# Optimization experiments

Measured on AMD Instinct MI355X. Metric: run time of the kernel, lower is better.

The kernel has to match this reference:

```python
import jax, jax.numpy as jnp
import numpy as np
from jax.scipy.special import logsumexp

S, L = 32768, 512  # seq_len, label_num


def setup_inputs() -> dict:
    key = jax.random.key(0)
    k1, k2, k3 = jax.random.split(key, 3)
    logit = jax.random.normal(k1, (S, L), dtype=jnp.float32)   # emissions [S, L]
    labels = jax.random.randint(k2, (S,), 0, L)                # gold path [S]
    T = jax.random.normal(k3, (L, L), dtype=jnp.float32)       # T[next, prev]
    return {"logit": logit, "labels": labels, "T": T}


def _crf_loss(logit, T, labels):
    # Forward algorithm: alpha_t[j] = logsumexp_i(alpha_{t-1}[i] + T[j, i]) + feat_t[j]
    alpha0 = logit[0]

    def step(alpha, feat):
        new_alpha = logsumexp(alpha[None, :] + T, axis=1) + feat  # [L]
        return new_alpha, None

    alpha_final, _ = jax.lax.scan(step, alpha0, logit[1:])
    log_Z = logsumexp(alpha_final)

    # Gold path score: feat_0[y0] + sum_{t>0} (feat_t[y_t] + T[y_t, y_{t-1}])
    emit = logit[0, labels[0]] + jnp.sum(logit[jnp.arange(1, logit.shape[0]), labels[1:]])
    trans = jnp.sum(T[labels[1:], labels[:-1]])
    gold = emit + trans
    return log_Z - gold


def reference(logit, labels, T):
    return _crf_loss(logit, T, labels)
```

## Files before the change

### kernel.cpp

```cpp
#include <hip/hip_runtime.h>
#include <stdint.h>


#define S_LEN 32768
#define L 512
#define CH 16
#define NCF 2048
#define NB  256
#define TPB 1024
#define LN448 6.104793232f
#define LN2   0.6931471806f

#define OFF_EAF  0
#define OFF_EAB  (256*1024)
#define OFF_G    (512*1024)
#define OFF_H    (OFF_G + 2048*512*2)
#define OFF_LSE  (OFF_H + 2048*512*2)
#define OFF_GOLD (OFF_LSE + 4104*4)
#define OFF_BAR  (OFF_GOLD + 1024)

#define PL_OFF   0
#define SP_OFF   16384
#define SR_OFF   17664
#define LF_OFF   18432
#define SMEM_TOTAL (18432 + 3*32768)

typedef float v4f __attribute__((ext_vector_type(4)));

__device__ __forceinline__ float b2f(unsigned short u){
  return __uint_as_float(((unsigned)u) << 16);
}
__device__ __forceinline__ unsigned short f2b(float x){
  unsigned u = __float_as_uint(x);
  return (unsigned short)((u + 0x7fffu + ((u >> 16) & 1u)) >> 16);
}
__device__ __forceinline__ unsigned char to_fp8(float v){
  int u = __builtin_amdgcn_cvt_pk_fp8_f32(v, v, 0, false);
  return (unsigned char)(u & 0xff);
}

__device__ __forceinline__ void stg_u8(unsigned char* p, unsigned char v){
  __hip_atomic_store(p, v, __ATOMIC_RELAXED, __HIP_MEMORY_SCOPE_AGENT);
}
__device__ __forceinline__ void stg_u64(unsigned long long* p, unsigned long long v){
  __hip_atomic_store(p, v, __ATOMIC_RELAXED, __HIP_MEMORY_SCOPE_AGENT);
}
__device__ __forceinline__ void stg_f32(float* p, float v){
  __hip_atomic_store(p, v, __ATOMIC_RELAXED, __HIP_MEMORY_SCOPE_AGENT);
}

__device__ __forceinline__ void gl2lds16(const void* g, void* l){
  __builtin_amdgcn_global_load_lds(
      (const __attribute__((address_space(1))) void*)g,
      (__attribute__((address_space(3))) void*)l, 16, 0, 0);
}

__device__ __forceinline__ void lds_sync(){
  asm volatile("s_waitcnt lgkmcnt(0)" ::: "memory");
  __builtin_amdgcn_sched_barrier(0);
  __builtin_amdgcn_s_barrier();
  __builtin_amdgcn_sched_barrier(0);
}
__device__ __forceinline__ void step_sync(){
  asm volatile("s_waitcnt vmcnt(2) lgkmcnt(0)" ::: "memory");
  __builtin_amdgcn_sched_barrier(0);
  __builtin_amdgcn_s_barrier();
  __builtin_amdgcn_sched_barrier(0);
}

__device__ __forceinline__ void grid_bar(unsigned* bar, unsigned target){
  __syncthreads();
  if (threadIdx.x == 0) {
    __hip_atomic_fetch_add(bar, 1u, __ATOMIC_RELAXED, __HIP_MEMORY_SCOPE_AGENT);
    unsigned it = 0;
    while (__hip_atomic_load(bar, __ATOMIC_RELAXED, __HIP_MEMORY_SCOPE_AGENT) < target) {
      __builtin_amdgcn_s_sleep(8);
      if ((++it & 255u) == 0u)
        (void)__hip_atomic_load(bar, __ATOMIC_ACQUIRE, __HIP_MEMORY_SCOPE_AGENT);
    }
    __builtin_amdgcn_fence(__ATOMIC_ACQUIRE, "agent");
  }
  __syncthreads();
}

__device__ __forceinline__ float blockSum(float v, float* sred){
  #pragma unroll
  for (int off = 32; off >= 1; off >>= 1) v += __shfl_xor(v, off);
  int wid = threadIdx.x >> 6, lane = threadIdx.x & 63;
  if (lane == 0) sred[wid] = v;
  __syncthreads();
  if (threadIdx.x < 16) {
    float t = sred[threadIdx.x];
    t += __shfl_xor(t, 8); t += __shfl_xor(t, 4);
    t += __shfl_xor(t, 2); t += __shfl_xor(t, 1);
    if (threadIdx.x == 0) sred[16] = t;
  }
  __syncthreads();
  float r = sred[16];
  __syncthreads();
  return r;
}

__device__ __forceinline__ float waveMax(float v){
  #pragma unroll
  for (int off = 32; off >= 1; off >>= 1) v = fmaxf(v, __shfl_xor(v, off));
  return v;
}
__device__ __forceinline__ float waveSum(float v){
  #pragma unroll
  for (int off = 32; off >= 1; off >>= 1) v += __shfl_xor(v, off);
  return v;
}

extern "C" __global__ __launch_bounds__(TPB, 4)
void crf_fused(const float* __restrict__ logit,
               const int* __restrict__ labels,
               const float* __restrict__ T,
               float* __restrict__ out,
               unsigned char* __restrict__ EAf,
               unsigned char* __restrict__ EAb,
               unsigned short* __restrict__ G,
               unsigned short* __restrict__ H,
               float* __restrict__ lsebuf,
               float* __restrict__ part,
               unsigned* __restrict__ bar){
  extern __shared__ __align__(16) char smem[];
  unsigned char* Pl = (unsigned char*)(smem + PL_OFF);
  float (*sPart)[20] = (float(*)[20])(smem + SP_OFF);
  float* sredG       = (float*)(smem + SR_OFF);
  char*  LF          = smem + LF_OFF;

  const int tidx = threadIdx.x;

  {
    int tid = blockIdx.x*TPB + tidx;
    int r    = tid & 7;
    int lane = (tid >> 3) & 63;
    int kt   = (tid >> 9) & 15;
    int R16  = tid >> 13;
    int j = R16*16 + (lane & 15);
    int i = kt*32 + ((lane >> 4) << 3) + r;
    stg_u8(EAf + tid, to_fp8(2.0f * __expf(T[j*L + i])));
    stg_u8(EAb + tid, to_fp8(2.0f * __expf(T[i*L + j])));
  }
  {
    float acc = 0.f;
    if (tidx < 128) {
      int t = blockIdx.x*128 + tidx;
      int yt = labels[t];
      float v = logit[(size_t)t*L + yt];
      if (t > 0) v += T[yt*L + labels[t-1]];
      acc = v;
    }
    float s = blockSum(acc, sredG);
    if (tidx == 0) stg_f32(part + blockIdx.x, s);
  }
  grid_bar(bar, NB);

  {
    const int w    = tidx >> 6;
    const int lane = tidx & 63;
    const int quad = lane >> 4;
    const int cl   = lane & 15;
    const bool fwd = (blockIdx.x < NB/2);
    const int  b   = fwd ? blockIdx.x : (blockIdx.x - NB/2);
    const int  cg  = fwd ? (b*16 + cl) : (1 + b*16 + cl);
    const int  cgc = min(cg, NCF-1);
    const bool isc0 = fwd && (cg == 0);
    const int  jrow0 = w*32 + quad*4;

    const int  cgw  = fwd ? (b*16 + w) : (1 + b*16 + w);
    const int  cgcw = min(cgw, NCF-1);
    const unsigned swzw = (unsigned)((w & 7) << 4);
    const unsigned so   = ((unsigned)(lane*16)) ^ swzw;

    const long* EAp = (const long*)(fwd ? EAf : EAb);
    long eA[2][16];
    #pragma unroll
    for (int mt = 0; mt < 2; ++mt)
      #pragma unroll
      for (int kt = 0; kt < 16; ++kt)
        eA[mt][kt] = EAp[(((w*2 + mt)*16) + kt)*64 + lane];

    int pladdr0, pladdr1;
    {
      int r0 = jrow0;
      pladdr0 = (r0 >> 5)*512 + ((((r0 >> 3) & 3)*16 + cl) << 3) + (r0 & 7);
      r0 = jrow0 + 16;
      pladdr1 = (r0 >> 5)*512 + ((((r0 >> 3) & 3)*16 + cl) << 3) + (r0 & 7);
    }
    const int bbbase = lane*8;
    const int scl = (cl & 7) << 4;
    const int ib  = w*128 + quad*16;
    const int fa0 = cl*2048 + (ib ^ scl);
    const int fa1 = cl*2048 + ((ib + 64) ^ scl);

    {
      size_t t0 = (size_t)(fwd ? (cgcw*CH + 0) : (cgcw*CH + CH - 2 - 0));
      size_t t1 = (size_t)(fwd ? (cgcw*CH + 1) : (cgcw*CH + CH - 2 - 1));
      const char* r0p = (const char*)logit + t0*(L*4);
      const char* r1p = (const char*)logit + t1*(L*4);
      char* d0 = LF + 0*32768 + w*2048;
      char* d1 = LF + 1*32768 + w*2048;
      gl2lds16(r0p + so, d0);  gl2lds16(r0p + 1024 + so, d0 + 1024);
      gl2lds16(r1p + so, d1);  gl2lds16(r1p + 1024 + so, d1 + 1024);
    }

    v4f v0, v1;
    if (fwd) {
      v0 = (v4f){1.f,1.f,1.f,1.f}; v1 = v0;
    } else {
      const float* ip = logit + (size_t)(cgc*CH + CH - 1)*L + jrow0;
      float4 x0 = *(const float4*)ip, x1 = *(const float4*)(ip + 16);
      v0 = (v4f){__expf(x0.x),__expf(x0.y),__expf(x0.z),__expf(x0.w)};
      v1 = (v4f){__expf(x1.x),__expf(x1.y),__expf(x1.z),__expf(x1.w)};
    }
    float m = 0.0f;
    int par = 0;
    int bo0 = 0, bo1 = 32768, bo2 = 2*32768;

    {
      float mx = fmaxf(fmaxf(fmaxf(v0[0],v0[1]),fmaxf(v0[2],v0[3])),
                       fmaxf(fmaxf(v1[0],v1[1]),fmaxf(v1[2],v1[3])));
      mx = fmaxf(mx, __shfl_xor(mx, 16));
      mx = fmaxf(mx, __shfl_xor(mx, 32));
      if (quad == 0) sPart[cl][w] = mx;
      lds_sync();
      const float4* sp4 = (const float4*)&sPart[cl][0];
      float4 q0 = sp4[0], q1 = sp4[1], q2 = sp4[2], q3 = sp4[3];
      float M = fmaxf(fmaxf(fmaxf(fmaxf(q0.x,q0.y),fmaxf(q0.z,q0.w)),
                            fmaxf(fmaxf(q1.x,q1.y),fmaxf(q1.z,q1.w))),
                      fmaxf(fmaxf(fmaxf(q2.x,q2.y),fmaxf(q2.z,q2.w)),
                            fmaxf(fmaxf(q3.x,q3.y),fmaxf(q3.z,q3.w))));
      float sc = 448.0f / M;
      int u0 = __builtin_amdgcn_cvt_pk_fp8_f32(v0[0]*sc, v0[1]*sc, 0, false);
      u0     = __builtin_amdgcn_cvt_pk_fp8_f32(v0[2]*sc, v0[3]*sc, u0, true);
      *(int*)&Pl[pladdr0] = u0;
      int u1 = __builtin_amdgcn_cvt_pk_fp8_f32(v1[0]*sc, v1[1]*sc, 0, false);
      u1     = __builtin_amdgcn_cvt_pk_fp8_f32(v1[2]*sc, v1[3]*sc, u1, true);
      *(int*)&Pl[pladdr1] = u1;
      m = __logf(M) - LN448;
      step_sync();
    }

    for (int k = 0; k < CH; ++k) {
      const bool last = (k == CH-1);
      const bool useF = fwd || !last;

      {
        const int ks = k + 2;
        const bool ok = fwd ? (ks <= CH-1) : (ks <= CH-2);
        if (ok) {
          size_t t = (size_t)(fwd ? (cgcw*CH + ks) : (cgcw*CH + CH - 2 - ks));
          const char* row = (const char*)logit + t*(L*4);
          char* dst = LF + bo2 + w*2048;
          gl2lds16(row + so, dst);
          gl2lds16(row + 1024 + so, dst + 1024);
        }
      }

      v4f a0 = (v4f){0.f,0.f,0.f,0.f};
      v4f a1 = (v4f){0.f,0.f,0.f,0.f};
      {
        const unsigned char* plr = Pl + par*8192 + bbbase;
        #pragma unroll
        for (int kt = 0; kt < 16; ++kt) {
          long bb = *(const long*)(plr + kt*512);
          a0 = __builtin_amdgcn_mfma_f32_16x16x32_fp8_fp8(eA[0][kt], bb, a0, 0, 0, 0);
          a1 = __builtin_amdgcn_mfma_f32_16x16x32_fp8_fp8(eA[1][kt], bb, a1, 0, 0, 0);
        }
      }

      if (useF) {
        const char* fb = LF + bo0;
        float4 q0 = *(const float4*)(fb + fa0);
        float4 q1 = *(const float4*)(fb + fa1);
        float f0=__expf(q0.x), f1=__expf(q0.y), f2=__expf(q0.z), f3=__expf(q0.w);
        float g0=__expf(q1.x), g1=__expf(q1.y), g2=__expf(q1.z), g3=__expf(q1.w);
        a0 = (v4f){a0[0]*f0, a0[1]*f1, a0[2]*f2, a0[3]*f3};
        a1 = (v4f){a1[0]*g0, a1[1]*g1, a1[2]*g2, a1[3]*g3};
        if (k == 0 && isc0) {
          a0 = (v4f){f0,f1,f2,f3}; a1 = (v4f){g0,g1,g2,g3}; m = 0.0f;
        }
      }

      if (last) {
        if (cg <= NCF-1) {
          float madj = m - (isc0 ? (float)(CH-1) : (float)CH) * LN2;
          unsigned short* dst = (fwd ? G : H) + (size_t)cg*L + jrow0;
          unsigned long long pv =
               (unsigned long long)f2b(__logf(a0[0]) + madj)
            | ((unsigned long long)f2b(__logf(a0[1]) + madj) << 16)
            | ((unsigned long long)f2b(__logf(a0[2]) + madj) << 32)
            | ((unsigned long long)f2b(__logf(a0[3]) + madj) << 48);
          stg_u64((unsigned long long*)dst, pv);
          pv = (unsigned long long)f2b(__logf(a1[0]) + madj)
            | ((unsigned long long)f2b(__logf(a1[1]) + madj) << 16)
            | ((unsigned long long)f2b(__logf(a1[2]) + madj) << 32)
            | ((unsigned long long)f2b(__logf(a1[3]) + madj) << 48);
          stg_u64((unsigned long long*)(dst + 16), pv);
        }
      } else {
        float mx = fmaxf(fmaxf(fmaxf(a0[0],a0[1]),fmaxf(a0[2],a0[3])),
                         fmaxf(fmaxf(a1[0],a1[1]),fmaxf(a1[2],a1[3])));
        mx = fmaxf(mx, __shfl_xor(mx, 16));
        mx = fmaxf(mx, __shfl_xor(mx, 32));
        if (quad == 0) sPart[cl][w] = mx;
        lds_sync();
        const float4* sp4 = (const float4*)&sPart[cl][0];
        float4 q0 = sp4[0], q1 = sp4[1], q2 = sp4[2], q3 = sp4[3];
        float M = fmaxf(fmaxf(fmaxf(fmaxf(q0.x,q0.y),fmaxf(q0.z,q0.w)),
                              fmaxf(fmaxf(q1.x,q1.y),fmaxf(q1.z,q1.w))),
                        fmaxf(fmaxf(fmaxf(q2.x,q2.y),fmaxf(q2.z,q2.w)),
                              fmaxf(fmaxf(q3.x,q3.y),fmaxf(q3.z,q3.w))));
        float sc = 448.0f / M;
        int u0 = __builtin_amdgcn_cvt_pk_fp8_f32(a0[0]*sc, a0[1]*sc, 0, false);
        u0     = __builtin_amdgcn_cvt_pk_fp8_f32(a0[2]*sc, a0[3]*sc, u0, true);
        *(int*)&Pl[(par^1)*8192 + pladdr0] = u0;
        int u1 = __builtin_amdgcn_cvt_pk_fp8_f32(a1[0]*sc, a1[1]*sc, 0, false);
        u1     = __builtin_amdgcn_cvt_pk_fp8_f32(a1[2]*sc, a1[3]*sc, u1, true);
        *(int*)&Pl[(par^1)*8192 + pladdr1] = u1;
        m += __logf(M) - LN448;
        step_sync();
        par ^= 1;
        int tmp = bo0; bo0 = bo1; bo1 = bo2; bo2 = tmp;
      }
    }
  }
  grid_bar(bar, 2*NB);

  if (blockIdx.x < 128) {
    const int w    = tidx >> 6;
    const int lane = tidx & 63;
    const int g    = blockIdx.x*16 + w;
    const int j8   = lane*8;
    if (g == 0) {
      const unsigned short* p = G + (size_t)(NCF-1)*L + j8;
      ushort4 a = *(const ushort4*)p, bq = *(const ushort4*)(p + 4);
      float v[8] = { b2f(a.x),b2f(a.y),b2f(a.z),b2f(a.w),
                     b2f(bq.x),b2f(bq.y),b2f(bq.z),b2f(bq.w) };
      float mx = v[0];
      #pragma unroll
      for (int r = 1; r < 8; ++r) mx = fmaxf(mx, v[r]);
      mx = waveMax(mx);
      float s = 0.f;
      #pragma unroll
      for (int r = 0; r < 8; ++r) s += __expf(v[r] - mx);
      s = waveSum(s);
      if (lane == 0) stg_f32(lsebuf + 2*NCF, mx + __logf(s));
    } else {
      const unsigned short* hp = H + (size_t)g*L + j8;
      const unsigned short* gp = G + (size_t)(g-1)*L + j8;
      ushort4 ha = *(const ushort4*)hp, hb = *(const ushort4*)(hp + 4);
      ushort4 ga = *(const ushort4*)gp, gb = *(const ushort4*)(gp + 4);
      float hv[8] = { b2f(ha.x),b2f(ha.y),b2f(ha.z),b2f(ha.w),
                      b2f(hb.x),b2f(hb.y),b2f(hb.z),b2f(hb.w) };
      float gv[8] = { b2f(ga.x),b2f(ga.y),b2f(ga.z),b2f(ga.w),
                      b2f(gb.x),b2f(gb.y),b2f(gb.z),b2f(gb.w) };
      float m1 = -3.0e38f, m2 = -3.0e38f;
      #pragma unroll
      for (int r = 0; r < 8; ++r) {
        float a = hv[r] + gv[r];
        m1 = fmaxf(m1, a); m2 = fmaxf(m2, hv[r]);
      }
      m1 = waveMax(m1); m2 = waveMax(m2);
      float s1 = 0.f, s2 = 0.f;
      #pragma unroll
      for (int r = 0; r < 8; ++r) {
        s1 += __expf(hv[r] + gv[r] - m1);
        s2 += __expf(hv[r] - m2);
      }
      s1 = waveSum(s1); s2 = waveSum(s2);
      if (lane == 0) {
        stg_f32(lsebuf + g,       m1 + __logf(s1));
        stg_f32(lsebuf + NCF + g, m2 + __logf(s2));
      }
    }
  }
  grid_bar(bar, 3*NB);

  if (blockIdx.x == 0) {
    float acc = 0.f;
    for (int c = tidx; c < NCF; c += TPB)
      if (c >= 1) acc += lsebuf[c] - lsebuf[NCF + c];
    if (tidx < NB) acc -= part[tidx];
    float s = blockSum(acc, sredG);
    if (tidx == 0) out[0] = lsebuf[2*NCF] + s;
  }
}

extern "C" void kernel_launch(void* const* d_in, const int* in_sizes, int n_in,
                              void* d_out, int out_size, void* d_ws, size_t ws_size,
                              hipStream_t stream){
  const float* logit = (const float*)d_in[0];
  const int* labels  = (const int*)d_in[1];
  const float* T     = (const float*)d_in[2];
  char* ws = (char*)d_ws;

  static bool attr_set = false;
  if (!attr_set) {
    hipFuncSetAttribute((const void*)crf_fused,
                        hipFuncAttributeMaxDynamicSharedMemorySize, SMEM_TOTAL);
    attr_set = true;
  }

  hipMemsetAsync(ws + OFF_BAR, 0, 64, stream);
  crf_fused<<<NB, TPB, SMEM_TOTAL, stream>>>(
      logit, labels, T, (float*)d_out,
      (unsigned char*)(ws + OFF_EAF), (unsigned char*)(ws + OFF_EAB),
      (unsigned short*)(ws + OFF_G), (unsigned short*)(ws + OFF_H),
      (float*)(ws + OFF_LSE), (float*)(ws + OFF_GOLD),
      (unsigned*)(ws + OFF_BAR));
}
```

Before: 156.5 us.

## Split persistent fused kernel into four launches, replacing software grid barriers

Breaks the single persistent kernel, which had atomic-spin grid barriers, into four kernels: prep, chunk scan, per-chunk LSE and final reduction. Stream ordering now provides the synchronisation, so the barrier memset, the spin loops and the agent-scope atomic stores go away in favour of plain stores. The cost is three extra launch gaps, and the chunk kernel has to reload its inputs from global memory in a fresh launch.

```diff
diff --git a/kernel.cpp b/kernel.cpp
--- a/kernel.cpp
+++ b/kernel.cpp
@@ -17,11 +17,9 @@
 #define OFF_H    (OFF_G + 2048*512*2)
 #define OFF_LSE  (OFF_H + 2048*512*2)
 #define OFF_GOLD (OFF_LSE + 4104*4)
-#define OFF_BAR  (OFF_GOLD + 1024)
 
 #define PL_OFF   0
 #define SP_OFF   16384
-#define SR_OFF   17664
 #define LF_OFF   18432
 #define SMEM_TOTAL (18432 + 3*32768)
 
@@ -37,16 +35,6 @@
 __device__ __forceinline__ unsigned char to_fp8(float v){
   int u = __builtin_amdgcn_cvt_pk_fp8_f32(v, v, 0, false);
   return (unsigned char)(u & 0xff);
-}
-
-__device__ __forceinline__ void stg_u8(unsigned char* p, unsigned char v){
-  __hip_atomic_store(p, v, __ATOMIC_RELAXED, __HIP_MEMORY_SCOPE_AGENT);
-}
-__device__ __forceinline__ void stg_u64(unsigned long long* p, unsigned long long v){
-  __hip_atomic_store(p, v, __ATOMIC_RELAXED, __HIP_MEMORY_SCOPE_AGENT);
-}
-__device__ __forceinline__ void stg_f32(float* p, float v){
-  __hip_atomic_store(p, v, __ATOMIC_RELAXED, __HIP_MEMORY_SCOPE_AGENT);
 }
 
 __device__ __forceinline__ void gl2lds16(const void* g, void* l){
@@ -68,22 +56,18 @@
   __builtin_amdgcn_sched_barrier(0);
 }
 
-__device__ __forceinline__ void grid_bar(unsigned* bar, unsigned target){
-  __syncthreads();
-  if (threadIdx.x == 0) {
-    __hip_atomic_fetch_add(bar, 1u, __ATOMIC_RELAXED, __HIP_MEMORY_SCOPE_AGENT);
-    unsigned it = 0;
-    while (__hip_atomic_load(bar, __ATOMIC_RELAXED, __HIP_MEMORY_SCOPE_AGENT) < target) {
-      __builtin_amdgcn_s_sleep(8);
-      if ((++it & 255u) == 0u)
-        (void)__hip_atomic_load(bar, __ATOMIC_ACQUIRE, __HIP_MEMORY_SCOPE_AGENT);
-    }
-    __builtin_amdgcn_fence(__ATOMIC_ACQUIRE, "agent");
-  }
-  __syncthreads();
-}
-
-__device__ __forceinline__ float blockSum(float v, float* sred){
+__device__ __forceinline__ float waveMax(float v){
+  #pragma unroll
+  for (int off = 32; off >= 1; off >>= 1) v = fmaxf(v, __shfl_xor(v, off));
+  return v;
+}
+__device__ __forceinline__ float waveSum(float v){
+  #pragma unroll
+  for (int off = 32; off >= 1; off >>= 1) v += __shfl_xor(v, off);
+  return v;
+}
+
+__device__ __forceinline__ float blockSum16(float v, float* sred){
   #pragma unroll
   for (int off = 32; off >= 1; off >>= 1) v += __shfl_xor(v, off);
   int wid = threadIdx.x >> 6, lane = threadIdx.x & 63;
@@ -100,38 +84,32 @@
   __syncthreads();
   return r;
 }
-
-__device__ __forceinline__ float waveMax(float v){
-  #pragma unroll
-  for (int off = 32; off >= 1; off >>= 1) v = fmaxf(v, __shfl_xor(v, off));
-  return v;
-}
-__device__ __forceinline__ float waveSum(float v){
+__device__ __forceinline__ float blockSum8(float v, float* sred){
   #pragma unroll
   for (int off = 32; off >= 1; off >>= 1) v += __shfl_xor(v, off);
-  return v;
-}
-
-extern "C" __global__ __launch_bounds__(TPB, 4)
-void crf_fused(const float* __restrict__ logit,
-               const int* __restrict__ labels,
-               const float* __restrict__ T,
-               float* __restrict__ out,
-               unsigned char* __restrict__ EAf,
-               unsigned char* __restrict__ EAb,
-               unsigned short* __restrict__ G,
-               unsigned short* __restrict__ H,
-               float* __restrict__ lsebuf,
-               float* __restrict__ part,
-               unsigned* __restrict__ bar){
-  extern __shared__ __align__(16) char smem[];
-  unsigned char* Pl = (unsigned char*)(smem + PL_OFF);
-  float (*sPart)[20] = (float(*)[20])(smem + SP_OFF);
-  float* sredG       = (float*)(smem + SR_OFF);
-  char*  LF          = smem + LF_OFF;
-
+  int wid = threadIdx.x >> 6, lane = threadIdx.x & 63;
+  if (lane == 0) sred[wid] = v;
+  __syncthreads();
+  if (threadIdx.x < 8) {
+    float t = sred[threadIdx.x];
+    t += __shfl_xor(t, 4); t += __shfl_xor(t, 2); t += __shfl_xor(t, 1);
+    if (threadIdx.x == 0) sred[8] = t;
+  }
+  __syncthreads();
+  float r = sred[8];
+  __syncthreads();
+  return r;
+}
+
+extern "C" __global__ __launch_bounds__(TPB)
+void crf_prep(const float* __restrict__ logit,
+              const int* __restrict__ labels,
+              const float* __restrict__ T,
+              unsigned char* __restrict__ EAf,
+              unsigned char* __restrict__ EAb,
+              float* __restrict__ part){
+  __shared__ float sredG[17];
   const int tidx = threadIdx.x;
-
   {
     int tid = blockIdx.x*TPB + tidx;
     int r    = tid & 7;
@@ -140,8 +118,8 @@
     int R16  = tid >> 13;
     int j = R16*16 + (lane & 15);
     int i = kt*32 + ((lane >> 4) << 3) + r;
-    stg_u8(EAf + tid, to_fp8(2.0f * __expf(T[j*L + i])));
-    stg_u8(EAb + tid, to_fp8(2.0f * __expf(T[i*L + j])));
+    EAf[tid] = to_fp8(2.0f * __expf(T[j*L + i]));
+    EAb[tid] = to_fp8(2.0f * __expf(T[i*L + j]));
   }
   {
     float acc = 0.f;
@@ -152,76 +130,168 @@
       if (t > 0) v += T[yt*L + labels[t-1]];
       acc = v;
     }
-    float s = blockSum(acc, sredG);
-    if (tidx == 0) stg_f32(part + blockIdx.x, s);
-  }
-  grid_bar(bar, NB);
-
+    float s = blockSum16(acc, sredG);
+    if (tidx == 0) part[blockIdx.x] = s;
+  }
+}
+
+extern "C" __global__ __launch_bounds__(TPB, 4)
+void crf_chunks(const float* __restrict__ logit,
+                const unsigned char* __restrict__ EAf,
+                const unsigned char* __restrict__ EAb,
+                unsigned short* __restrict__ G,
+                unsigned short* __restrict__ H){
+  extern __shared__ __align__(16) char smem[];
+  unsigned char* Pl  = (unsigned char*)(smem + PL_OFF);
+  float (*sPart)[20] = (float(*)[20])(smem + SP_OFF);
+  char*  LF          = smem + LF_OFF;
+
+  const int tidx = threadIdx.x;
+  const int w    = tidx >> 6;
+  const int lane = tidx & 63;
+  const int quad = lane >> 4;
+  const int cl   = lane & 15;
+  const bool fwd = (blockIdx.x < NB/2);
+  const int  b   = fwd ? blockIdx.x : (blockIdx.x - NB/2);
+  const int  cg  = fwd ? (b*16 + cl) : (1 + b*16 + cl);
+  const int  cgc = min(cg, NCF-1);
+  const bool isc0 = fwd && (cg == 0);
+  const int  jrow0 = w*32 + quad*4;
+
+  const int  cgw  = fwd ? (b*16 + w) : (1 + b*16 + w);
+  const int  cgcw = min(cgw, NCF-1);
+  const unsigned swzw = (unsigned)((w & 7) << 4);
+  const unsigned so   = ((unsigned)(lane*16)) ^ swzw;
+
+  const long* EAp = (const long*)(fwd ? EAf : EAb);
+  long eA[2][16];
+  #pragma unroll
+  for (int mt = 0; mt < 2; ++mt)
+    #pragma unroll
+    for (int kt = 0; kt < 16; ++kt)
+      eA[mt][kt] = EAp[(((w*2 + mt)*16) + kt)*64 + lane];
+
+  int pladdr0, pladdr1;
   {
-    const int w    = tidx >> 6;
-    const int lane = tidx & 63;
-    const int quad = lane >> 4;
-    const int cl   = lane & 15;
-    const bool fwd = (blockIdx.x < NB/2);
-    const int  b   = fwd ? blockIdx.x : (blockIdx.x - NB/2);
-    const int  cg  = fwd ? (b*16 + cl) : (1 + b*16 + cl);
-    const int  cgc = min(cg, NCF-1);
-    const bool isc0 = fwd && (cg == 0);
-    const int  jrow0 = w*32 + quad*4;
-
-    const int  cgw  = fwd ? (b*16 + w) : (1 + b*16 + w);
-    const int  cgcw = min(cgw, NCF-1);
-    const unsigned swzw = (unsigned)((w & 7) << 4);
-    const unsigned so   = ((unsigned)(lane*16)) ^ swzw;
-
-    const long* EAp = (const long*)(fwd ? EAf : EAb);
-    long eA[2][16];
-    #pragma unroll
-    for (int mt = 0; mt < 2; ++mt)
+    int r0 = jrow0;
+    pladdr0 = (r0 >> 5)*512 + ((((r0 >> 3) & 3)*16 + cl) << 3) + (r0 & 7);
+    r0 = jrow0 + 16;
+    pladdr1 = (r0 >> 5)*512 + ((((r0 >> 3) & 3)*16 + cl) << 3) + (r0 & 7);
+  }
+  const int bbbase = lane*8;
+  const int scl = (cl & 7) << 4;
+  const int ib  = w*128 + quad*16;
+  const int fa0 = cl*2048 + (ib ^ scl);
+  const int fa1 = cl*2048 + ((ib + 64) ^ scl);
+
+  {
+    size_t t0 = (size_t)(fwd ? (cgcw*CH + 0) : (cgcw*CH + CH - 2 - 0));
+    size_t t1 = (size_t)(fwd ? (cgcw*CH + 1) : (cgcw*CH + CH - 2 - 1));
+    const char* r0p = (const char*)logit + t0*(L*4);
+    const char* r1p = (const char*)logit + t1*(L*4);
+    char* d0 = LF + 0*32768 + w*2048;
+    char* d1 = LF + 1*32768 + w*2048;
+    gl2lds16(r0p + so, d0);  gl2lds16(r0p + 1024 + so, d0 + 1024);
+    gl2lds16(r1p + so, d1);  gl2lds16(r1p + 1024 + so, d1 + 1024);
+  }
+
+  v4f v0, v1;
+  if (fwd) {
+    v0 = (v4f){1.f,1.f,1.f,1.f}; v1 = v0;
+  } else {
+    const float* ip = logit + (size_t)(cgc*CH + CH - 1)*L + jrow0;
+    float4 x0 = *(const float4*)ip, x1 = *(const float4*)(ip + 16);
+    v0 = (v4f){__expf(x0.x),__expf(x0.y),__expf(x0.z),__expf(x0.w)};
+    v1 = (v4f){__expf(x1.x),__expf(x1.y),__expf(x1.z),__expf(x1.w)};
+  }
+  float m = 0.0f;
+  int par = 0;
+  int bo0 = 0, bo1 = 32768, bo2 = 2*32768;
+
+  {
+    float mx = fmaxf(fmaxf(fmaxf(v0[0],v0[1]),fmaxf(v0[2],v0[3])),
+                     fmaxf(fmaxf(v1[0],v1[1]),fmaxf(v1[2],v1[3])));
+    mx = fmaxf(mx, __shfl_xor(mx, 16));
+    mx = fmaxf(mx, __shfl_xor(mx, 32));
+    if (quad == 0) sPart[cl][w] = mx;
+    lds_sync();
+    const float4* sp4 = (const float4*)&sPart[cl][0];
+    float4 q0 = sp4[0], q1 = sp4[1], q2 = sp4[2], q3 = sp4[3];
+    float M = fmaxf(fmaxf(fmaxf(fmaxf(q0.x,q0.y),fmaxf(q0.z,q0.w)),
+                          fmaxf(fmaxf(q1.x,q1.y),fmaxf(q1.z,q1.w))),
+                    fmaxf(fmaxf(fmaxf(q2.x,q2.y),fmaxf(q2.z,q2.w)),
+                          fmaxf(fmaxf(q3.x,q3.y),fmaxf(q3.z,q3.w))));
+    float sc = 448.0f / M;
+    int u0 = __builtin_amdgcn_cvt_pk_fp8_f32(v0[0]*sc, v0[1]*sc, 0, false);
+    u0     = __builtin_amdgcn_cvt_pk_fp8_f32(v0[2]*sc, v0[3]*sc, u0, true);
+    *(int*)&Pl[pladdr0] = u0;
+    int u1 = __builtin_amdgcn_cvt_pk_fp8_f32(v1[0]*sc, v1[1]*sc, 0, false);
+    u1     = __builtin_amdgcn_cvt_pk_fp8_f32(v1[2]*sc, v1[3]*sc, u1, true);
+    *(int*)&Pl[pladdr1] = u1;
+    m = __logf(M) - LN448;
+    step_sync();
+  }
+
+  for (int k = 0; k < CH; ++k) {
+    const bool last = (k == CH-1);
+    const bool useF = fwd || !last;
+
+    {
+      const int ks = k + 2;
+      const bool ok = fwd ? (ks <= CH-1) : (ks <= CH-2);
+      if (ok) {
+        size_t t = (size_t)(fwd ? (cgcw*CH + ks) : (cgcw*CH + CH - 2 - ks));
+        const char* row = (const char*)logit + t*(L*4);
+        char* dst = LF + bo2 + w*2048;
+        gl2lds16(row + so, dst);
+        gl2lds16(row + 1024 + so, dst + 1024);
+      }
+    }
+
+    v4f a0 = (v4f){0.f,0.f,0.f,0.f};
+    v4f a1 = (v4f){0.f,0.f,0.f,0.f};
+    {
+      const unsigned char* plr = Pl + par*8192 + bbbase;
       #pragma unroll
-      for (int kt = 0; kt < 16; ++kt)
-        eA[mt][kt] = EAp[(((w*2 + mt)*16) + kt)*64 + lane];
-
-    int pladdr0, pladdr1;
-    {
-      int r0 = jrow0;
-      pladdr0 = (r0 >> 5)*512 + ((((r0 >> 3) & 3)*16 + cl) << 3) + (r0 & 7);
-      r0 = jrow0 + 16;
-      pladdr1 = (r0 >> 5)*512 + ((((r0 >> 3) & 3)*16 + cl) << 3) + (r0 & 7);
-    }
-    const int bbbase = lane*8;
-    const int scl = (cl & 7) << 4;
-    const int ib  = w*128 + quad*16;
-    const int fa0 = cl*2048 + (ib ^ scl);
-    const int fa1 = cl*2048 + ((ib + 64) ^ scl);
-
-    {
-      size_t t0 = (size_t)(fwd ? (cgcw*CH + 0) : (cgcw*CH + CH - 2 - 0));
-      size_t t1 = (size_t)(fwd ? (cgcw*CH + 1) : (cgcw*CH + CH - 2 - 1));
-      const char* r0p = (const char*)logit + t0*(L*4);
-      const char* r1p = (const char*)logit + t1*(L*4);
-      char* d0 = LF + 0*32768 + w*2048;
-      char* d1 = LF + 1*32768 + w*2048;
-      gl2lds16(r0p + so, d0);  gl2lds16(r0p + 1024 + so, d0 + 1024);
-      gl2lds16(r1p + so, d1);  gl2lds16(r1p + 1024 + so, d1 + 1024);
-    }
-
-    v4f v0, v1;
-    if (fwd) {
-      v0 = (v4f){1.f,1.f,1.f,1.f}; v1 = v0;
+      for (int kt = 0; kt < 16; ++kt) {
+        long bb = *(const long*)(plr + kt*512);
+        a0 = __builtin_amdgcn_mfma_f32_16x16x32_fp8_fp8(eA[0][kt], bb, a0, 0, 0, 0);
+        a1 = __builtin_amdgcn_mfma_f32_16x16x32_fp8_fp8(eA[1][kt], bb, a1, 0, 0, 0);
+      }
+    }
+
+    if (useF) {
+      const char* fb = LF + bo0;
+      float4 q0 = *(const float4*)(fb + fa0);
+      float4 q1 = *(const float4*)(fb + fa1);
+      float f0=__expf(q0.x), f1=__expf(q0.y), f2=__expf(q0.z), f3=__expf(q0.w);
+      float g0=__expf(q1.x), g1=__expf(q1.y), g2=__expf(q1.z), g3=__expf(q1.w);
+      a0 = (v4f){a0[0]*f0, a0[1]*f1, a0[2]*f2, a0[3]*f3};
+      a1 = (v4f){a1[0]*g0, a1[1]*g1, a1[2]*g2, a1[3]*g3};
+      if (k == 0 && isc0) {
+        a0 = (v4f){f0,f1,f2,f3}; a1 = (v4f){g0,g1,g2,g3}; m = 0.0f;
+      }
+    }
+
+    if (last) {
+      if (cg <= NCF-1) {
+        float madj = m - (isc0 ? (float)(CH-1) : (float)CH) * LN2;
+        unsigned short* dst = (fwd ? G : H) + (size_t)cg*L + jrow0;
+        unsigned long long pv =
+             (unsigned long long)f2b(__logf(a0[0]) + madj)
+          | ((unsigned long long)f2b(__logf(a0[1]) + madj) << 16)
+          | ((unsigned long long)f2b(__logf(a0[2]) + madj) << 32)
+          | ((unsigned long long)f2b(__logf(a0[3]) + madj) << 48);
+        *(unsigned long long*)dst = pv;
+        pv = (unsigned long long)f2b(__logf(a1[0]) + madj)
+          | ((unsigned long long)f2b(__logf(a1[1]) + madj) << 16)
+          | ((unsigned long long)f2b(__logf(a1[2]) + madj) << 32)
+          | ((unsigned long long)f2b(__logf(a1[3]) + madj) << 48);
+        *(unsigned long long*)(dst + 16) = pv;
+      }
     } else {
-      const float* ip = logit + (size_t)(cgc*CH + CH - 1)*L + jrow0;
-      float4 x0 = *(const float4*)ip, x1 = *(const float4*)(ip + 16);
-      v0 = (v4f){__expf(x0.x),__expf(x0.y),__expf(x0.z),__expf(x0.w)};
-      v1 = (v4f){__expf(x1.x),__expf(x1.y),__expf(x1.z),__expf(x1.w)};
-    }
-    float m = 0.0f;
-    int par = 0;
-    int bo0 = 0, bo1 = 32768, bo2 = 2*32768;
-
-    {
-      float mx = fmaxf(fmaxf(fmaxf(v0[0],v0[1]),fmaxf(v0[2],v0[3])),
-                       fmaxf(fmaxf(v1[0],v1[1]),fmaxf(v1[2],v1[3])));
+      float mx = fmaxf(fmaxf(fmaxf(a0[0],a0[1]),fmaxf(a0[2],a0[3])),
+                       fmaxf(fmaxf(a1[0],a1[1]),fmaxf(a1[2],a1[3])));
       mx = fmaxf(mx, __shfl_xor(mx, 16));
       mx = fmaxf(mx, __shfl_xor(mx, 32));
       if (quad == 0) sPart[cl][w] = mx;
@@ -233,160 +303,86 @@
                       fmaxf(fmaxf(fmaxf(q2.x,q2.y),fmaxf(q2.z,q2.w)),
                             fmaxf(fmaxf(q3.x,q3.y),fmaxf(q3.z,q3.w))));
       float sc = 448.0f / M;
-      int u0 = __builtin_amdgcn_cvt_pk_fp8_f32(v0[0]*sc, v0[1]*sc, 0, false);
-      u0     = __builtin_amdgcn_cvt_pk_fp8_f32(v0[2]*sc, v0[3]*sc, u0, true);
-      *(int*)&Pl[pladdr0] = u0;
-      int u1 = __builtin_amdgcn_cvt_pk_fp8_f32(v1[0]*sc, v1[1]*sc, 0, false);
-      u1     = __builtin_amdgcn_cvt_pk_fp8_f32(v1[2]*sc, v1[3]*sc, u1, true);
-      *(int*)&Pl[pladdr1] = u1;
-      m = __logf(M) - LN448;
+      int u0 = __builtin_amdgcn_cvt_pk_fp8_f32(a0[0]*sc, a0[1]*sc, 0, false);
+      u0     = __builtin_amdgcn_cvt_pk_fp8_f32(a0[2]*sc, a0[3]*sc, u0, true);
+      *(int*)&Pl[(par^1)*8192 + pladdr0] = u0;
+      int u1 = __builtin_amdgcn_cvt_pk_fp8_f32(a1[0]*sc, a1[1]*sc, 0, false);
+      u1     = __builtin_amdgcn_cvt_pk_fp8_f32(a1[2]*sc, a1[3]*sc, u1, true);
+      *(int*)&Pl[(par^1)*8192 + pladdr1] = u1;
+      m += __logf(M) - LN448;
       step_sync();
-    }
-
-    for (int k = 0; k < CH; ++k) {
-      const bool last = (k == CH-1);
-      const bool useF = fwd || !last;
-
-      {
-        const int ks = k + 2;
-        const bool ok = fwd ? (ks <= CH-1) : (ks <= CH-2);
-        if (ok) {
-          size_t t = (size_t)(fwd ? (cgcw*CH + ks) : (cgcw*CH + CH - 2 - ks));
-          const char* row = (const char*)logit + t*(L*4);
-          char* dst = LF + bo2 + w*2048;
-          gl2lds16(row + so, dst);
-          gl2lds16(row + 1024 + so, dst + 1024);
-        }
-      }
-
-      v4f a0 = (v4f){0.f,0.f,0.f,0.f};
-      v4f a1 = (v4f){0.f,0.f,0.f,0.f};
-      {
-        const unsigned char* plr = Pl + par*8192 + bbbase;
-        #pragma unroll
-        for (int kt = 0; kt < 16; ++kt) {
-          long bb = *(const long*)(plr + kt*512);
-          a0 = __builtin_amdgcn_mfma_f32_16x16x32_fp8_fp8(eA[0][kt], bb, a0, 0, 0, 0);
-          a1 = __builtin_amdgcn_mfma_f32_16x16x32_fp8_fp8(eA[1][kt], bb, a1, 0, 0, 0);
-        }
-      }
-
-      if (useF) {
-        const char* fb = LF + bo0;
-        float4 q0 = *(const float4*)(fb + fa0);
-        float4 q1 = *(const float4*)(fb + fa1);
-        float f0=__expf(q0.x), f1=__expf(q0.y), f2=__expf(q0.z), f3=__expf(q0.w);
-        float g0=__expf(q1.x), g1=__expf(q1.y), g2=__expf(q1.z), g3=__expf(q1.w);
-        a0 = (v4f){a0[0]*f0, a0[1]*f1, a0[2]*f2, a0[3]*f3};
-        a1 = (v4f){a1[0]*g0, a1[1]*g1, a1[2]*g2, a1[3]*g3};
-        if (k == 0 && isc0) {
-          a0 = (v4f){f0,f1,f2,f3}; a1 = (v4f){g0,g1,g2,g3}; m = 0.0f;
-        }
-      }
-
-      if (last) {
-        if (cg <= NCF-1) {
-          float madj = m - (isc0 ? (float)(CH-1) : (float)CH) * LN2;
-          unsigned short* dst = (fwd ? G : H) + (size_t)cg*L + jrow0;
-          unsigned long long pv =
-               (unsigned long long)f2b(__logf(a0[0]) + madj)
-            | ((unsigned long long)f2b(__logf(a0[1]) + madj) << 16)
-            | ((unsigned long long)f2b(__logf(a0[2]) + madj) << 32)
-            | ((unsigned long long)f2b(__logf(a0[3]) + madj) << 48);
-          stg_u64((unsigned long long*)dst, pv);
-          pv = (unsigned long long)f2b(__logf(a1[0]) + madj)
-            | ((unsigned long long)f2b(__logf(a1[1]) + madj) << 16)
-            | ((unsigned long long)f2b(__logf(a1[2]) + madj) << 32)
-            | ((unsigned long long)f2b(__logf(a1[3]) + madj) << 48);
-          stg_u64((unsigned long long*)(dst + 16), pv);
-        }
-      } else {
-        float mx = fmaxf(fmaxf(fmaxf(a0[0],a0[1]),fmaxf(a0[2],a0[3])),
-                         fmaxf(fmaxf(a1[0],a1[1]),fmaxf(a1[2],a1[3])));
-        mx = fmaxf(mx, __shfl_xor(mx, 16));
-        mx = fmaxf(mx, __shfl_xor(mx, 32));
-        if (quad == 0) sPart[cl][w] = mx;
-        lds_sync();
-        const float4* sp4 = (const float4*)&sPart[cl][0];
-        float4 q0 = sp4[0], q1 = sp4[1], q2 = sp4[2], q3 = sp4[3];
-        float M = fmaxf(fmaxf(fmaxf(fmaxf(q0.x,q0.y),fmaxf(q0.z,q0.w)),
-                              fmaxf(fmaxf(q1.x,q1.y),fmaxf(q1.z,q1.w))),
-                        fmaxf(fmaxf(fmaxf(q2.x,q2.y),fmaxf(q2.z,q2.w)),
-                              fmaxf(fmaxf(q3.x,q3.y),fmaxf(q3.z,q3.w))));
-        float sc = 448.0f / M;
-        int u0 = __builtin_amdgcn_cvt_pk_fp8_f32(a0[0]*sc, a0[1]*sc, 0, false);
-        u0     = __builtin_amdgcn_cvt_pk_fp8_f32(a0[2]*sc, a0[3]*sc, u0, true);
-        *(int*)&Pl[(par^1)*8192 + pladdr0] = u0;
-        int u1 = __builtin_amdgcn_cvt_pk_fp8_f32(a1[0]*sc, a1[1]*sc, 0, false);
-        u1     = __builtin_amdgcn_cvt_pk_fp8_f32(a1[2]*sc, a1[3]*sc, u1, true);
-        *(int*)&Pl[(par^1)*8192 + pladdr1] = u1;
-        m += __logf(M) - LN448;
-        step_sync();
-        par ^= 1;
-        int tmp = bo0; bo0 = bo1; bo1 = bo2; bo2 = tmp;
-      }
-    }
-  }
-  grid_bar(bar, 2*NB);
-
-  if (blockIdx.x < 128) {
-    const int w    = tidx >> 6;
-    const int lane = tidx & 63;
-    const int g    = blockIdx.x*16 + w;
-    const int j8   = lane*8;
-    if (g == 0) {
-      const unsigned short* p = G + (size_t)(NCF-1)*L + j8;
-      ushort4 a = *(const ushort4*)p, bq = *(const ushort4*)(p + 4);
-      float v[8] = { b2f(a.x),b2f(a.y),b2f(a.z),b2f(a.w),
-                     b2f(bq.x),b2f(bq.y),b2f(bq.z),b2f(bq.w) };
-      float mx = v[0];
-      #pragma unroll
-      for (int r = 1; r < 8; ++r) mx = fmaxf(mx, v[r]);
-      mx = waveMax(mx);
-      float s = 0.f;
-      #pragma unroll
-      for (int r = 0; r < 8; ++r) s += __expf(v[r] - mx);
-      s = waveSum(s);
-      if (lane == 0) stg_f32(lsebuf + 2*NCF, mx + __logf(s));
-    } else {
-      const unsigned short* hp = H + (size_t)g*L + j8;
-      const unsigned short* gp = G + (size_t)(g-1)*L + j8;
-      ushort4 ha = *(const ushort4*)hp, hb = *(const ushort4*)(hp + 4);
-      ushort4 ga = *(const ushort4*)gp, gb = *(const ushort4*)(gp + 4);
-      float hv[8] = { b2f(ha.x),b2f(ha.y),b2f(ha.z),b2f(ha.w),
-                      b2f(hb.x),b2f(hb.y),b2f(hb.z),b2f(hb.w) };
-      float gv[8] = { b2f(ga.x),b2f(ga.y),b2f(ga.z),b2f(ga.w),
-                      b2f(gb.x),b2f(gb.y),b2f(gb.z),b2f(gb.w) };
-      float m1 = -3.0e38f, m2 = -3.0e38f;
-      #pragma unroll
-      for (int r = 0; r < 8; ++r) {
-        float a = hv[r] + gv[r];
-        m1 = fmaxf(m1, a); m2 = fmaxf(m2, hv[r]);
-      }
-      m1 = waveMax(m1); m2 = waveMax(m2);
-      float s1 = 0.f, s2 = 0.f;
-      #pragma unroll
-      for (int r = 0; r < 8; ++r) {
-        s1 += __expf(hv[r] + gv[r] - m1);
-        s2 += __expf(hv[r] - m2);
-      }
-      s1 = waveSum(s1); s2 = waveSum(s2);
-      if (lane == 0) {
-        stg_f32(lsebuf + g,       m1 + __logf(s1));
-        stg_f32(lsebuf + NCF + g, m2 + __logf(s2));
-      }
-    }
-  }
-  grid_bar(bar, 3*NB);
-
-  if (blockIdx.x == 0) {
-    float acc = 0.f;
-    for (int c = tidx; c < NCF; c += TPB)
-      if (c >= 1) acc += lsebuf[c] - lsebuf[NCF + c];
-    if (tidx < NB) acc -= part[tidx];
-    float s = blockSum(acc, sredG);
-    if (tidx == 0) out[0] = lsebuf[2*NCF] + s;
-  }
+      par ^= 1;
+      int tmp = bo0; bo0 = bo1; bo1 = bo2; bo2 = tmp;
+    }
+  }
+}
+
+extern "C" __global__ __launch_bounds__(512)
+void crf_lse(const unsigned short* __restrict__ G,
+             const unsigned short* __restrict__ H,
+             float* __restrict__ lsebuf){
+  const int tidx = threadIdx.x;
+  const int w    = tidx >> 6;
+  const int lane = tidx & 63;
+  const int g    = blockIdx.x*8 + w;
+  const int j8   = lane*8;
+  if (g == 0) {
+    const unsigned short* p = G + (size_t)(NCF-1)*L + j8;
+    ushort4 a = *(const ushort4*)p, bq = *(const ushort4*)(p + 4);
+    float v[8] = { b2f(a.x),b2f(a.y),b2f(a.z),b2f(a.w),
+                   b2f(bq.x),b2f(bq.y),b2f(bq.z),b2f(bq.w) };
+    float mx = v[0];
+    #pragma unroll
+    for (int r = 1; r < 8; ++r) mx = fmaxf(mx, v[r]);
+    mx = waveMax(mx);
+    float s = 0.f;
+    #pragma unroll
+    for (int r = 0; r < 8; ++r) s += __expf(v[r] - mx);
+    s = waveSum(s);
+    if (lane == 0) lsebuf[2*NCF] = mx + __logf(s);
+  } else {
+    const unsigned short* hp = H + (size_t)g*L + j8;
+    const unsigned short* gp = G + (size_t)(g-1)*L + j8;
+    ushort4 ha = *(const ushort4*)hp, hb = *(const ushort4*)(hp + 4);
+    ushort4 ga = *(const ushort4*)gp, gb = *(const ushort4*)(gp + 4);
+    float hv[8] = { b2f(ha.x),b2f(ha.y),b2f(ha.z),b2f(ha.w),
+                    b2f(hb.x),b2f(hb.y),b2f(hb.z),b2f(hb.w) };
+    float gv[8] = { b2f(ga.x),b2f(ga.y),b2f(ga.z),b2f(ga.w),
+                    b2f(gb.x),b2f(gb.y),b2f(gb.z),b2f(gb.w) };
+    float m1 = -3.0e38f, m2 = -3.0e38f;
+    #pragma unroll
+    for (int r = 0; r < 8; ++r) {
+      float a = hv[r] + gv[r];
+      m1 = fmaxf(m1, a); m2 = fmaxf(m2, hv[r]);
+    }
+    m1 = waveMax(m1); m2 = waveMax(m2);
+    float s1 = 0.f, s2 = 0.f;
+    #pragma unroll
+    for (int r = 0; r < 8; ++r) {
+      s1 += __expf(hv[r] + gv[r] - m1);
+      s2 += __expf(hv[r] - m2);
+    }
+    s1 = waveSum(s1); s2 = waveSum(s2);
+    if (lane == 0) {
+      lsebuf[g]       = m1 + __logf(s1);
+      lsebuf[NCF + g] = m2 + __logf(s2);
+    }
+  }
+}
+
+extern "C" __global__ __launch_bounds__(512)
+void crf_final(const float* __restrict__ lsebuf,
+               const float* __restrict__ part,
+               float* __restrict__ out){
+  __shared__ float sredG[9];
+  const int tidx = threadIdx.x;
+  float acc = 0.f;
+  #pragma unroll
+  for (int c = tidx; c < NCF; c += 512)
+    if (c >= 1) acc += lsebuf[c] - lsebuf[NCF + c];
+  if (tidx < NB) acc -= part[tidx];
+  float s = blockSum8(acc, sredG);
+  if (tidx == 0) out[0] = lsebuf[2*NCF] + s;
 }
 
 extern "C" void kernel_launch(void* const* d_in, const int* in_sizes, int n_in,
@@ -395,20 +391,24 @@
   const float* logit = (const float*)d_in[0];
   const int* labels  = (const int*)d_in[1];
   const float* T     = (const float*)d_in[2];
+  float* out = (float*)d_out;
   char* ws = (char*)d_ws;
+  unsigned char* EAf = (unsigned char*)(ws + OFF_EAF);
+  unsigned char* EAb = (unsigned char*)(ws + OFF_EAB);
+  unsigned short* G  = (unsigned short*)(ws + OFF_G);
+  unsigned short* H  = (unsigned short*)(ws + OFF_H);
+  float* lsebuf = (float*)(ws + OFF_LSE);
+  float* part   = (float*)(ws + OFF_GOLD);
 
   static bool attr_set = false;
   if (!attr_set) {
-    hipFuncSetAttribute((const void*)crf_fused,
+    (void)hipFuncSetAttribute((const void*)crf_chunks,
                         hipFuncAttributeMaxDynamicSharedMemorySize, SMEM_TOTAL);
     attr_set = true;
   }
 
-  hipMemsetAsync(ws + OFF_BAR, 0, 64, stream);
-  crf_fused<<<NB, TPB, SMEM_TOTAL, stream>>>(
-      logit, labels, T, (float*)d_out,
-      (unsigned char*)(ws + OFF_EAF), (unsigned char*)(ws + OFF_EAB),
-      (unsigned short*)(ws + OFF_G), (unsigned short*)(ws + OFF_H),
-      (float*)(ws + OFF_LSE), (float*)(ws + OFF_GOLD),
-      (unsigned*)(ws + OFF_BAR));
-}
+  crf_prep  <<<NB, TPB, 0, stream>>>(logit, labels, T, EAf, EAb, part);
+  crf_chunks<<<NB, TPB, SMEM_TOTAL, stream>>>(logit, EAf, EAb, G, H);
+  crf_lse   <<<NB, 512, 0, stream>>>(G, H, lsebuf);
+  crf_final <<<1, 512, 0, stream>>>(lsebuf, part, out);
+}
```

New measurement: 131.9 us. 15.7% less time.
